# Kernel tuning notes

Measured on AMD Instinct MI355X. Metric: run time of the kernel, lower is better.

The kernel has to match this reference:

```python
import jax, jax.numpy as jnp
import numpy as np

EPS = 1e-6
MAX_ITER = 3

def skew(w):
    z = jnp.zeros_like(w[:, 0])
    return jnp.stack([
        jnp.stack([z, -w[:, 2], w[:, 1]], -1),
        jnp.stack([w[:, 2], z, -w[:, 0]], -1),
        jnp.stack([-w[:, 1], w[:, 0], z], -1)], -2)

def twist2mat(w):
    # Rodrigues formula, w: [B,3] -> R: [B,3,3]
    theta = jnp.linalg.norm(w, axis=-1, keepdims=True) + 1e-12
    axis = w / theta
    Km = skew(axis)
    th = theta[..., None]
    I = jnp.eye(3, dtype=w.dtype)
    return I + jnp.sin(th) * Km + (1.0 - jnp.cos(th)) * (Km @ Km)

def sobel_gradient(img, normalize=True):
    # replicate-pad + 3x3 Sobel, img: [B,C,H,W]
    p = jnp.pad(img, ((0, 0), (0, 0), (1, 1), (1, 1)), mode='edge')
    tl = p[..., :-2, :-2]; tc = p[..., :-2, 1:-1]; tr = p[..., :-2, 2:]
    ml = p[..., 1:-1, :-2]; mr = p[..., 1:-1, 2:]
    bl = p[..., 2:, :-2]; bc = p[..., 2:, 1:-1]; br = p[..., 2:, 2:]
    dx = (tr - tl) + 2.0 * (mr - ml) + (br - bl)
    dy = (bl - tl) + 2.0 * (bc - tc) + (br - tr)
    if normalize:
        mag = jnp.sqrt(dx * dx + dy * dy + 1e-8)
        dx, dy = dx / mag, dy / mag
    return dx, dy

def _bilinear_one(F, u, v):
    # F: [C,H,W]; u,v: [H,W] pixel coords; border padding (grid_sample-like)
    C, H, W = F.shape
    u = jnp.clip(u, 0.0, W - 1.0)
    v = jnp.clip(v, 0.0, H - 1.0)
    x0 = jnp.floor(u); y0 = jnp.floor(v)
    wx = u - x0; wy = v - y0
    x0i = x0.astype(jnp.int32); y0i = y0.astype(jnp.int32)
    x1i = jnp.minimum(x0i + 1, W - 1); y1i = jnp.minimum(y0i + 1, H - 1)
    g = lambda yi, xi: F[:, yi, xi]  # advanced-index gather -> [C,H,W]
    return (g(y0i, x0i) * (1 - wx) * (1 - wy) + g(y0i, x1i) * wx * (1 - wy)
            + g(y1i, x0i) * (1 - wx) * wy + g(y1i, x1i) * wx * wy)

def warp_features(F, u, v):
    # F: [B,C,H,W]; u,v: [B,1,H,W]
    return jax.vmap(_bilinear_one)(F, u[:, 0], v[:, 0])

def generate_xy_grid(B, H, W, K):
    fx, fy, cx, cy = [K[:, i].reshape(B, 1, 1, 1) for i in range(4)]
    uu, vv = jnp.meshgrid(jnp.arange(W, dtype=K.dtype), jnp.arange(H, dtype=K.dtype))
    px = (uu[None, None] - cx) / fx
    py = (vv[None, None] - cy) / fy
    return px, py  # [B,1,H,W] each

def batch_warp_inverse_depth(px, py, invD0, R, t, K):
    B, _, H, W = px.shape
    xy1 = jnp.concatenate([px, py, jnp.ones_like(px)], 1).reshape(B, 3, -1)
    warped = R @ xy1 + t[:, :, None] * invD0.reshape(B, 1, -1)
    x_, y_, s_ = warped[:, 0], warped[:, 1], warped[:, 2]
    fx, fy, cx, cy = [K[:, i].reshape(B, 1) for i in range(4)]
    u_ = (x_ / s_ * fx + cx).reshape(B, 1, H, W)
    v_ = (y_ / s_ * fy + cy).reshape(B, 1, H, W)
    inv_z = invD0 / s_.reshape(B, 1, H, W)
    return u_, v_, inv_z

def check_occ(inv_z_buffer, invD1, u, v, thres=0.1):
    B, _, H, W = invD1.shape
    inv_z_warped = warp_features(invD1, u, v)
    inlier = inv_z_buffer > inv_z_warped - thres
    inview = (u > 0) & (u < W) & (v > 0) & (v < H)
    return ~(inlier & inview)  # [B,1,H,W] bool

def compute_jacobian_warping(invD, K, px, py):
    # linearized at origin (pose=None branch)
    B, _, H, W = invD.shape
    x = px.reshape(B, -1); y = py.reshape(B, -1); d = invD.reshape(B, -1)
    O = jnp.zeros_like(x)
    xy = x * y
    dx_dp = jnp.stack([-xy, 1.0 + x * x, -y, d, O, -d * x], -1)
    dy_dp = jnp.stack([-(1.0 + y * y), xy, x, O, d, -d * y], -1)
    fx = K[:, 0].reshape(B, 1, 1); fy = K[:, 1].reshape(B, 1, 1)
    return dx_dp * fx, dy_dp * fy  # [B,HW,6] each

def lev_mar_H(JtWJ):
    diag = jnp.eye(6, dtype=JtWJ.dtype)
    trace = jnp.trace(JtWJ, axis1=1, axis2=2)
    return JtWJ + (trace * 1e-6)[:, None, None] * diag

def forward(twist0, x0, x1, invD0, invD1, sigma0, sigma1, K):
    B, C, H, W = x0.shape
    N = H * W
    dtype = x0.dtype
    R = twist2mat(twist0[:, :3])
    t = twist0[:, 3:]
    px, py = generate_xy_grid(B, H, W, K)
    # inverse-compositional: template Jacobian precomputed once
    Jf_x, Jf_y = sobel_gradient(x0, normalize=True)
    Jx_p, Jy_p = compute_jacobian_warping(invD0, K, px, py)
    J = (Jf_x.reshape(B, C, N, 1) * Jx_p.reshape(B, 1, N, 6)
         + Jf_y.reshape(B, C, N, 1) * Jy_p.reshape(B, 1, N, 6))  # [B,C,N,6]
    for _ in range(MAX_ITER):
        u_w, v_w, inv_z = batch_warp_inverse_depth(px, py, invD0, R, t, K)
        occ = check_occ(inv_z, invD1, u_w, v_w)
        f_r = warp_features(x1, u_w, v_w)
        sigma_r = warp_features(sigma1, u_w, v_w)
        res = f_r - x0
        sigma = jnp.sqrt(sigma_r * sigma_r + sigma0 * sigma0)
        wres = jnp.where(occ, EPS, res / sigma)  # [B,C,H,W]
        valid = (~occ).reshape(B, 1, N, 1).astype(dtype)
        Jw = (J / sigma.reshape(B, C, N, 1) * valid).reshape(B, C * N, 6)
        r = jnp.where(occ, 0.0, wres).reshape(B, C * N)
        JtWJ = jnp.einsum('bnk,bnl->bkl', Jw, Jw)
        Rhs = jnp.einsum('bnk,bn->bk', Jw, r)[..., None]
        xi = jnp.linalg.solve(lev_mar_H(JtWJ), Rhs)  # [B,6,1]
        d_R = twist2mat(-xi[:, :3, 0])
        d_t = -(d_R @ xi[:, 3:])
        t = (R @ d_t)[:, :, 0] + t
        R = R @ d_R
    return jnp.concatenate([R.reshape(B, 9), t], axis=1)  # [B,12]

def setup_inputs() -> dict:
    key = jax.random.key(0)
    ks = jax.random.split(key, 7)
    B, C, H, W = 8, 16, 240, 320
    twist0 = jax.random.normal(ks[0], (B, 6), jnp.float32) * 0.01
    x0 = jax.random.normal(ks[1], (B, C, H, W), jnp.float32)
    x1 = jax.random.normal(ks[2], (B, C, H, W), jnp.float32)
    invD0 = jax.random.uniform(ks[3], (B, 1, H, W), jnp.float32, 0.1, 1.0)
    invD1 = jax.random.uniform(ks[4], (B, 1, H, W), jnp.float32, 0.1, 1.0)
    sigma0 = jax.random.uniform(ks[5], (B, C, H, W), jnp.float32, 0.1, 1.0)
    sigma1 = jax.random.uniform(ks[6], (B, C, H, W), jnp.float32, 0.1, 1.0)
    Kmat = jnp.tile(jnp.array([[0.8 * W, 0.8 * W, W / 2.0, H / 2.0]], jnp.float32), (B, 1))
    return dict(twist0=twist0, x0=x0, x1=x1, invD0=invD0, invD1=invD1,
                sigma0=sigma0, sigma1=sigma1, K=Kmat)

def reference(twist0, x0, x1, invD0, invD1, sigma0, sigma1, K):
    return forward(twist0, x0, x1, invD0, invD1, sigma0, sigma1, K)
```

## Files before the change

kernel.cpp:

```cpp
#include <hip/hip_runtime.h>
#include <hip/hip_fp16.h>

#define B_ 8
#define C_ 16
#define H_ 240
#define W_ 320
#define N_ (H_*W_)

__device__ __forceinline__ void twist2mat_dev(float w0, float w1, float w2, float R[9]) {
    float th = sqrtf(w0*w0 + w1*w1 + w2*w2) + 1e-12f;
    float ax = w0/th, ay = w1/th, az = w2/th;
    float s = sinf(th), c = cosf(th), ic = 1.0f - c;
    R[0] = 1.0f + ic*(ax*ax - 1.0f);
    R[1] = -s*az + ic*ax*ay;
    R[2] =  s*ay + ic*ax*az;
    R[3] =  s*az + ic*ax*ay;
    R[4] = 1.0f + ic*(ay*ay - 1.0f);
    R[5] = -s*ax + ic*ay*az;
    R[6] = -s*ay + ic*ax*az;
    R[7] =  s*ax + ic*ay*az;
    R[8] = 1.0f + ic*(az*az - 1.0f);
}

__device__ __forceinline__ unsigned pack_h2(float a, float b) {
    __half2 h = __floats2half2_rn(a, b);
    return *reinterpret_cast<unsigned*>(&h);
}
__device__ __forceinline__ float2 unpack_h2(unsigned u) {
    __half2 h = *reinterpret_cast<__half2*>(&u);
    return __half22float2(h);
}

__device__ __forceinline__ void solve_update(const float* __restrict__ ac, float R[9], float t[3]) {
    float M[6][7];
    {
        int idx = 0;
        #pragma unroll
        for (int k = 0; k < 6; k++)
            #pragma unroll
            for (int l = k; l < 6; l++) { M[k][l] = ac[idx]; M[l][k] = ac[idx]; idx++; }
    }
    const float trace = M[0][0]+M[1][1]+M[2][2]+M[3][3]+M[4][4]+M[5][5];
    const float lam = trace * 1e-6f;
    #pragma unroll
    for (int i = 0; i < 6; i++) { M[i][i] += lam; M[i][6] = ac[21+i]; }

    #pragma unroll
    for (int k = 0; k < 6; k++) {
        const float inv = 1.0f / M[k][k];
        #pragma unroll
        for (int i = k+1; i < 6; i++) {
            const float f = M[i][k] * inv;
            #pragma unroll
            for (int j = k; j < 7; j++) M[i][j] -= f * M[k][j];
        }
    }
    float xi[6];
    #pragma unroll
    for (int i = 5; i >= 0; i--) {
        float s = M[i][6];
        #pragma unroll
        for (int j = i+1; j < 6; j++) s -= M[i][j]*xi[j];
        xi[i] = s / M[i][i];
    }

    float dR[9];
    twist2mat_dev(-xi[0], -xi[1], -xi[2], dR);
    const float dt0 = -(dR[0]*xi[3] + dR[1]*xi[4] + dR[2]*xi[5]);
    const float dt1 = -(dR[3]*xi[3] + dR[4]*xi[4] + dR[5]*xi[5]);
    const float dt2 = -(dR[6]*xi[3] + dR[7]*xi[4] + dR[8]*xi[5]);

    const float nt0 = R[0]*dt0 + R[1]*dt1 + R[2]*dt2 + t[0];
    const float nt1 = R[3]*dt0 + R[4]*dt1 + R[5]*dt2 + t[1];
    const float nt2 = R[6]*dt0 + R[7]*dt1 + R[8]*dt2 + t[2];
    float nR[9];
    #pragma unroll
    for (int i = 0; i < 3; i++)
        #pragma unroll
        for (int j = 0; j < 3; j++)
            nR[i*3+j] = R[i*3+0]*dR[0*3+j] + R[i*3+1]*dR[1*3+j] + R[i*3+2]*dR[2*3+j];
    #pragma unroll
    for (int i = 0; i < 9; i++) R[i] = nR[i];
    t[0] = nt0; t[1] = nt1; t[2] = nt2;
}

__device__ __forceinline__ void build_RT(const float* __restrict__ twist0,
                                         const float* __restrict__ accum,
                                         int b, int iters, float R[9], float t[3]) {
    const float* w = twist0 + b*6;
    twist2mat_dev(w[0], w[1], w[2], R);
    t[0] = w[3]; t[1] = w[4]; t[2] = w[5];
    for (int j = 0; j < iters; j++)
        solve_update(accum + (size_t)(j*B_ + b)*27, R, t);
}

__launch_bounds__(256)
__global__ void precompute_kernel(const float* __restrict__ x0, const float* __restrict__ x1,
                                  const float* __restrict__ sigma0, const float* __restrict__ sigma1,
                                  uint4* __restrict__ P0h, uint4* __restrict__ X1S1h,
                                  float* __restrict__ accum)
{
    if (blockIdx.x == 0 && blockIdx.y == 0 && blockIdx.z == 0) {
        for (int k = threadIdx.x; k < 3*B_*27; k += 256) accum[k] = 0.0f;
    }
    const int pix = blockIdx.x*256 + threadIdx.x;
    const int cg = blockIdx.y;
    const int b = blockIdx.z;
    const int h = pix / W_, w = pix - h*W_;
    const int hm = max(h-1,0), hp = min(h+1,H_-1);
    const int wm = max(w-1,0), wp = min(w+1,W_-1);

    unsigned p0[8];
    unsigned xsp[4];
    #pragma unroll
    for (int i = 0; i < 4; i++) {
        const int c = cg*4 + i;
        const size_t base = ((size_t)(b*C_+c))*N_;
        const float* xc = x0 + base;
        const float tl = xc[hm*W_+wm], tc_ = xc[hm*W_+w], tr = xc[hm*W_+wp];
        const float ml = xc[h*W_+wm],                     mr = xc[h*W_+wp];
        const float bl = xc[hp*W_+wm], bc_ = xc[hp*W_+w], br = xc[hp*W_+wp];
        const float dx = tr - tl + 2.0f*(mr - ml) + (br - bl);
        const float dy = bl - tl + 2.0f*(bc_ - tc_) + (br - tr);
        const float mag = sqrtf(dx*dx + dy*dy + 1e-8f);
        const float s0v = sigma0[base + pix];
        p0[i*2+0] = pack_h2(dx/mag, dy/mag);
        p0[i*2+1] = pack_h2(xc[pix], s0v*s0v);
        xsp[i] = pack_h2(x1[base + pix], sigma1[base + pix]);
    }
    uint4 a; a.x = p0[0]; a.y = p0[1]; a.z = p0[2]; a.w = p0[3];
    uint4 bb; bb.x = p0[4]; bb.y = p0[5]; bb.z = p0[6]; bb.w = p0[7];
    P0h[((size_t)(b*8 + cg*2  ))*N_ + pix] = a;
    P0h[((size_t)(b*8 + cg*2+1))*N_ + pix] = bb;
    uint4 q; q.x = xsp[0]; q.y = xsp[1]; q.z = xsp[2]; q.w = xsp[3];
    X1S1h[((size_t)(b*4 + cg))*N_ + pix] = q;
}

__launch_bounds__(256)
__global__ void iter_kernel(const uint4* __restrict__ P0h, const uint4* __restrict__ X1S1h,
                            const float* __restrict__ invD0, const float* __restrict__ invD1,
                            const float* __restrict__ Kmat, const float* __restrict__ twist0,
                            float* __restrict__ accum, int it)
{
    const int b = blockIdx.y;
    const int pix = blockIdx.x * 256 + threadIdx.x;
    const int h = pix / W_;
    const int w = pix - h*W_;

    float Rm[9], tv[3];
    build_RT(twist0, accum, b, it, Rm, tv);

    const float fx = Kmat[b*4+0], fy = Kmat[b*4+1], cx = Kmat[b*4+2], cy = Kmat[b*4+3];

    float acc[27];
    #pragma unroll
    for (int j = 0; j < 27; j++) acc[j] = 0.0f;

    const float px = ((float)w - cx) / fx;
    const float py = ((float)h - cy) / fy;
    const float d  = invD0[b*N_ + pix];

    const float x_ = Rm[0]*px + Rm[1]*py + Rm[2] + tv[0]*d;
    const float y_ = Rm[3]*px + Rm[4]*py + Rm[5] + tv[1]*d;
    const float s_ = Rm[6]*px + Rm[7]*py + Rm[8] + tv[2]*d;
    const float u = x_/s_*fx + cx;
    const float v = y_/s_*fy + cy;
    const float inv_z = d / s_;

    const float uc = fminf(fmaxf(u, 0.0f), (float)(W_-1));
    const float vc = fminf(fmaxf(v, 0.0f), (float)(H_-1));
    const float x0f = floorf(uc), y0f = floorf(vc);
    const float wx = uc - x0f, wy = vc - y0f;
    const int x0i = (int)x0f, y0i = (int)y0f;
    const int x1i = min(x0i+1, W_-1), y1i = min(y0i+1, H_-1);
    const float w00 = (1.0f-wx)*(1.0f-wy), w01 = wx*(1.0f-wy);
    const float w10 = (1.0f-wx)*wy,        w11 = wx*wy;
    const int i00 = y0i*W_+x0i, i01 = y0i*W_+x1i, i10 = y1i*W_+x0i, i11 = y1i*W_+x1i;

    const float* dz = invD1 + b*N_;
    const float zw = dz[i00]*w00 + dz[i01]*w01 + dz[i10]*w10 + dz[i11]*w11;
    const bool inlier = inv_z > zw - 0.1f;
    const bool inview = (u > 0.0f) && (u < (float)W_) && (v > 0.0f) && (v < (float)H_);
    const bool valid  = inlier && inview;

    if (valid) {
        const float xy = px*py;
        const float Av[6] = { -xy*fx, (1.0f+px*px)*fx, -py*fx, d*fx, 0.0f, -d*px*fx };
        const float Bv[6] = { -(1.0f+py*py)*fy, xy*fy, px*fy, 0.0f, d*fy, -d*py*fy };

        float Swxx=0.f, Swxy=0.f, Swyy=0.f, Srx=0.f, Sry=0.f;
        const uint4* P0b   = P0h   + (size_t)b*8*N_;
        const uint4* X1S1b = X1S1h + (size_t)b*4*N_;

#define CH(gword, xword, t00, t01, t10, t11) { \
        const float2 g  = unpack_h2(gword); \
        const float2 xs = unpack_h2(xword); \
        const float2 a00 = unpack_h2(t00), a01 = unpack_h2(t01), \
                     a10 = unpack_h2(t10), a11 = unpack_h2(t11); \
        const float fr = a00.x*w00 + a01.x*w01 + a10.x*w10 + a11.x*w11; \
        const float sr = a00.y*w00 + a01.y*w01 + a10.y*w10 + a11.y*w11; \
        const float inv_s2 = 1.0f/(sr*sr + xs.y); \
        const float res = fr - xs.x; \
        const float gxw = g.x*inv_s2, gyw = g.y*inv_s2; \
        Swxx += g.x*gxw; Swxy += g.x*gyw; Swyy += g.y*gyw; \
        Srx  += res*gxw; Sry  += res*gyw; }

        #pragma unroll
        for (int cg = 0; cg < 4; cg++) {
            const uint4 pA = P0b[(size_t)(cg*2  )*N_ + pix];
            const uint4 pB = P0b[(size_t)(cg*2+1)*N_ + pix];
            const uint4* xsb = X1S1b + (size_t)cg*N_;
            const uint4 q00 = xsb[i00], q01 = xsb[i01], q10 = xsb[i10], q11 = xsb[i11];
            CH(pA.x, pA.y, q00.x, q01.x, q10.x, q11.x)
            CH(pA.z, pA.w, q00.y, q01.y, q10.y, q11.y)
            CH(pB.x, pB.y, q00.z, q01.z, q10.z, q11.z)
            CH(pB.z, pB.w, q00.w, q01.w, q10.w, q11.w)
        }
#undef CH

        int idx = 0;
        #pragma unroll
        for (int k = 0; k < 6; k++) {
            #pragma unroll
            for (int l = k; l < 6; l++) {
                acc[idx++] = Swxx*Av[k]*Av[l] + Swxy*(Av[k]*Bv[l] + Bv[k]*Av[l]) + Swyy*Bv[k]*Bv[l];
            }
        }
        #pragma unroll
        for (int k = 0; k < 6; k++) acc[21+k] = Srx*Av[k] + Sry*Bv[k];
    }

    const int lane = threadIdx.x & 63;
    const int wave = threadIdx.x >> 6;
    __shared__ float red[4][27];
    #pragma unroll
    for (int j = 0; j < 27; j++) {
        float vv = acc[j];
        vv += __shfl_down(vv, 32);
        vv += __shfl_down(vv, 16);
        vv += __shfl_down(vv, 8);
        vv += __shfl_down(vv, 4);
        vv += __shfl_down(vv, 2);
        vv += __shfl_down(vv, 1);
        if (lane == 0) red[wave][j] = vv;
    }
    __syncthreads();
    if (threadIdx.x < 27) {
        float s = red[0][threadIdx.x] + red[1][threadIdx.x] + red[2][threadIdx.x] + red[3][threadIdx.x];
        atomicAdd(&accum[(size_t)(it*B_ + b)*27 + threadIdx.x], s);
    }
}

__global__ void finalize_kernel(const float* __restrict__ twist0, const float* __restrict__ accum,
                                float* __restrict__ out)
{
    const int b = threadIdx.x;
    if (b >= B_) return;
    float Rm[9], tv[3];
    build_RT(twist0, accum, b, 3, Rm, tv);
    float* ob = out + b*12;
    #pragma unroll
    for (int i = 0; i < 9; i++) ob[i] = Rm[i];
    ob[9] = tv[0]; ob[10] = tv[1]; ob[11] = tv[2];
}

extern "C" void kernel_launch(void* const* d_in, const int* in_sizes, int n_in,
                              void* d_out, int out_size, void* d_ws, size_t ws_size,
                              hipStream_t stream) {
    const float* twist0 = (const float*)d_in[0];
    const float* x0     = (const float*)d_in[1];
    const float* x1     = (const float*)d_in[2];
    const float* invD0  = (const float*)d_in[3];
    const float* invD1  = (const float*)d_in[4];
    const float* sigma0 = (const float*)d_in[5];
    const float* sigma1 = (const float*)d_in[6];
    const float* Kmat   = (const float*)d_in[7];
    float* out = (float*)d_out;

    const size_t p0_bytes = (size_t)B_*8*N_*sizeof(uint4);
    const size_t xs_bytes = (size_t)B_*4*N_*sizeof(uint4);

    uint4* P0h   = (uint4*)d_ws;
    uint4* X1S1h = (uint4*)((char*)d_ws + p0_bytes);
    float* accum = (float*)((char*)d_ws + p0_bytes + xs_bytes);

    hipLaunchKernelGGL(precompute_kernel, dim3(N_/256, 4, B_), dim3(256), 0, stream,
                       x0, x1, sigma0, sigma1, P0h, X1S1h, accum);

    dim3 grid(N_/256, B_);
    for (int it = 0; it < 3; ++it) {
        hipLaunchKernelGGL(iter_kernel, grid, dim3(256), 0, stream,
                           P0h, X1S1h, invD0, invD1, Kmat, twist0, accum, it);
    }
    hipLaunchKernelGGL(finalize_kernel, dim3(1), dim3(64), 0, stream, twist0, accum, out);
}
```

Before: 362.1 us.

## Solve pose update in last block via ticket counter, drop per-block rebuild

```diff
diff --git a/kernel.cpp b/kernel.cpp
--- a/kernel.cpp
+++ b/kernel.cpp
@@ -6,6 +6,7 @@
 #define H_ 240
 #define W_ 320
 #define N_ (H_*W_)
+#define ITER_BLOCKS_PER_B (N_/256)
 
 __device__ __forceinline__ void twist2mat_dev(float w0, float w1, float w2, float R[9]) {
     float th = sqrtf(w0*w0 + w1*w1 + w2*w2) + 1e-12f;
@@ -31,19 +32,19 @@
     return __half22float2(h);
 }
 
-__device__ __forceinline__ void solve_update(const float* __restrict__ ac, float R[9], float t[3]) {
+__device__ __forceinline__ void solve_update(const float* sums, float R[9], float t[3]) {
     float M[6][7];
     {
         int idx = 0;
         #pragma unroll
         for (int k = 0; k < 6; k++)
             #pragma unroll
-            for (int l = k; l < 6; l++) { M[k][l] = ac[idx]; M[l][k] = ac[idx]; idx++; }
+            for (int l = k; l < 6; l++) { M[k][l] = sums[idx]; M[l][k] = sums[idx]; idx++; }
     }
     const float trace = M[0][0]+M[1][1]+M[2][2]+M[3][3]+M[4][4]+M[5][5];
     const float lam = trace * 1e-6f;
     #pragma unroll
-    for (int i = 0; i < 6; i++) { M[i][i] += lam; M[i][6] = ac[21+i]; }
+    for (int i = 0; i < 6; i++) { M[i][i] += lam; M[i][6] = sums[21+i]; }
 
     #pragma unroll
     for (int k = 0; k < 6; k++) {
@@ -84,24 +85,26 @@
     t[0] = nt0; t[1] = nt1; t[2] = nt2;
 }
 
-__device__ __forceinline__ void build_RT(const float* __restrict__ twist0,
-                                         const float* __restrict__ accum,
-                                         int b, int iters, float R[9], float t[3]) {
-    const float* w = twist0 + b*6;
-    twist2mat_dev(w[0], w[1], w[2], R);
-    t[0] = w[3]; t[1] = w[4]; t[2] = w[5];
-    for (int j = 0; j < iters; j++)
-        solve_update(accum + (size_t)(j*B_ + b)*27, R, t);
-}
-
 __launch_bounds__(256)
 __global__ void precompute_kernel(const float* __restrict__ x0, const float* __restrict__ x1,
                                   const float* __restrict__ sigma0, const float* __restrict__ sigma1,
+                                  const float* __restrict__ twist0,
                                   uint4* __restrict__ P0h, uint4* __restrict__ X1S1h,
-                                  float* __restrict__ accum)
+                                  float* __restrict__ accum, float* __restrict__ RTbuf,
+                                  unsigned* __restrict__ tickets)
 {
     if (blockIdx.x == 0 && blockIdx.y == 0 && blockIdx.z == 0) {
         for (int k = threadIdx.x; k < 3*B_*27; k += 256) accum[k] = 0.0f;
+        if (threadIdx.x >= 64 && threadIdx.x < 64 + 3*B_) tickets[threadIdx.x - 64] = 0u;
+        if (threadIdx.x < B_) {
+            const float* w = twist0 + threadIdx.x*6;
+            float R[9];
+            twist2mat_dev(w[0], w[1], w[2], R);
+            float* rt = RTbuf + (size_t)threadIdx.x*12;
+            #pragma unroll
+            for (int i = 0; i < 9; i++) rt[i] = R[i];
+            rt[9] = w[3]; rt[10] = w[4]; rt[11] = w[5];
+        }
     }
     const int pix = blockIdx.x*256 + threadIdx.x;
     const int cg = blockIdx.y;
@@ -110,8 +113,7 @@
     const int hm = max(h-1,0), hp = min(h+1,H_-1);
     const int wm = max(w-1,0), wp = min(w+1,W_-1);
 
-    unsigned p0[8];
-    unsigned xsp[4];
+    unsigned p0[8], xsp[4];
     #pragma unroll
     for (int i = 0; i < 4; i++) {
         const int c = cg*4 + i;
@@ -139,30 +141,29 @@
 __launch_bounds__(256)
 __global__ void iter_kernel(const uint4* __restrict__ P0h, const uint4* __restrict__ X1S1h,
                             const float* __restrict__ invD0, const float* __restrict__ invD1,
-                            const float* __restrict__ Kmat, const float* __restrict__ twist0,
-                            float* __restrict__ accum, int it)
+                            const float* __restrict__ Kmat,
+                            float* __restrict__ accum, float* __restrict__ RTbuf,
+                            unsigned* __restrict__ tickets, float* __restrict__ out, int it)
 {
     const int b = blockIdx.y;
-    const int pix = blockIdx.x * 256 + threadIdx.x;
+    const int pix = blockIdx.x*256 + threadIdx.x;
+    const int tid = threadIdx.x;
     const int h = pix / W_;
     const int w = pix - h*W_;
 
-    float Rm[9], tv[3];
-    build_RT(twist0, accum, b, it, Rm, tv);
-
+    const float* rt = RTbuf + (size_t)(it*B_ + b)*12;
+    const float R00=rt[0],R01=rt[1],R02=rt[2],R10=rt[3],R11=rt[4],R12=rt[5],
+                R20=rt[6],R21=rt[7],R22=rt[8];
+    const float t0=rt[9], t1=rt[10], t2=rt[11];
     const float fx = Kmat[b*4+0], fy = Kmat[b*4+1], cx = Kmat[b*4+2], cy = Kmat[b*4+3];
-
-    float acc[27];
-    #pragma unroll
-    for (int j = 0; j < 27; j++) acc[j] = 0.0f;
 
     const float px = ((float)w - cx) / fx;
     const float py = ((float)h - cy) / fy;
-    const float d  = invD0[b*N_ + pix];
-
-    const float x_ = Rm[0]*px + Rm[1]*py + Rm[2] + tv[0]*d;
-    const float y_ = Rm[3]*px + Rm[4]*py + Rm[5] + tv[1]*d;
-    const float s_ = Rm[6]*px + Rm[7]*py + Rm[8] + tv[2]*d;
+    const float d  = invD0[(size_t)b*N_ + pix];
+
+    const float x_ = R00*px + R01*py + R02 + t0*d;
+    const float y_ = R10*px + R11*py + R12 + t1*d;
+    const float s_ = R20*px + R21*py + R22 + t2*d;
     const float u = x_/s_*fx + cx;
     const float v = y_/s_*fy + cy;
     const float inv_z = d / s_;
@@ -177,13 +178,16 @@
     const float w10 = (1.0f-wx)*wy,        w11 = wx*wy;
     const int i00 = y0i*W_+x0i, i01 = y0i*W_+x1i, i10 = y1i*W_+x0i, i11 = y1i*W_+x1i;
 
-    const float* dz = invD1 + b*N_;
+    const float* dz = invD1 + (size_t)b*N_;
     const float zw = dz[i00]*w00 + dz[i01]*w01 + dz[i10]*w10 + dz[i11]*w11;
     const bool inlier = inv_z > zw - 0.1f;
     const bool inview = (u > 0.0f) && (u < (float)W_) && (v > 0.0f) && (v < (float)H_);
-    const bool valid  = inlier && inview;
-
-    if (valid) {
+
+    float acc[27];
+    #pragma unroll
+    for (int j = 0; j < 27; j++) acc[j] = 0.0f;
+
+    if (inlier && inview) {
         const float xy = px*py;
         const float Av[6] = { -xy*fx, (1.0f+px*px)*fx, -py*fx, d*fx, 0.0f, -d*px*fx };
         const float Bv[6] = { -(1.0f+py*py)*fy, xy*fy, px*fy, 0.0f, d*fy, -d*py*fy };
@@ -205,11 +209,11 @@
         Swxx += g.x*gxw; Swxy += g.x*gyw; Swyy += g.y*gyw; \
         Srx  += res*gxw; Sry  += res*gyw; }
 
-        #pragma unroll
-        for (int cg = 0; cg < 4; cg++) {
-            const uint4 pA = P0b[(size_t)(cg*2  )*N_ + pix];
-            const uint4 pB = P0b[(size_t)(cg*2+1)*N_ + pix];
-            const uint4* xsb = X1S1b + (size_t)cg*N_;
+        #pragma unroll 2
+        for (int cgi = 0; cgi < 4; cgi++) {
+            const uint4 pA = P0b[(size_t)(cgi*2  )*N_ + pix];
+            const uint4 pB = P0b[(size_t)(cgi*2+1)*N_ + pix];
+            const uint4* xsb = X1S1b + (size_t)cgi*N_;
             const uint4 q00 = xsb[i00], q01 = xsb[i01], q10 = xsb[i10], q11 = xsb[i11];
             CH(pA.x, pA.y, q00.x, q01.x, q10.x, q11.x)
             CH(pA.z, pA.w, q00.y, q01.y, q10.y, q11.y)
@@ -230,9 +234,9 @@
         for (int k = 0; k < 6; k++) acc[21+k] = Srx*Av[k] + Sry*Bv[k];
     }
 
-    const int lane = threadIdx.x & 63;
-    const int wave = threadIdx.x >> 6;
     __shared__ float red[4][27];
+    const int lane = tid & 63;
+    const int wave = tid >> 6;
     #pragma unroll
     for (int j = 0; j < 27; j++) {
         float vv = acc[j];
@@ -245,23 +249,42 @@
         if (lane == 0) red[wave][j] = vv;
     }
     __syncthreads();
-    if (threadIdx.x < 27) {
-        float s = red[0][threadIdx.x] + red[1][threadIdx.x] + red[2][threadIdx.x] + red[3][threadIdx.x];
-        atomicAdd(&accum[(size_t)(it*B_ + b)*27 + threadIdx.x], s);
-    }
-}
-
-__global__ void finalize_kernel(const float* __restrict__ twist0, const float* __restrict__ accum,
-                                float* __restrict__ out)
-{
-    const int b = threadIdx.x;
-    if (b >= B_) return;
-    float Rm[9], tv[3];
-    build_RT(twist0, accum, b, 3, Rm, tv);
-    float* ob = out + b*12;
-    #pragma unroll
-    for (int i = 0; i < 9; i++) ob[i] = Rm[i];
-    ob[9] = tv[0]; ob[10] = tv[1]; ob[11] = tv[2];
+    float* ac = accum + (size_t)(it*B_ + b)*27;
+    if (tid < 27) {
+        float s = red[0][tid] + red[1][tid] + red[2][tid] + red[3][tid];
+        atomicAdd(&ac[tid], s);
+    }
+    __syncthreads();
+
+    __shared__ unsigned lastFlag;
+    if (tid == 0) {
+        __threadfence();
+        unsigned prev = atomicAdd(&tickets[it*B_ + b], 1u);
+        lastFlag = (prev == ITER_BLOCKS_PER_B - 1) ? 1u : 0u;
+    }
+    __syncthreads();
+
+    if (lastFlag && tid < 64) {
+        __threadfence();
+        float sv = 0.0f;
+        if (tid < 27) sv = atomicAdd(&ac[tid], 0.0f);
+        float sums[27];
+        #pragma unroll
+        for (int j = 0; j < 27; j++) sums[j] = __shfl(sv, j);
+
+        float R[9], t[3];
+        #pragma unroll
+        for (int i = 0; i < 9; i++) R[i] = rt[i];
+        t[0] = rt[9]; t[1] = rt[10]; t[2] = rt[11];
+        solve_update(sums, R, t);
+
+        if (tid == 0) {
+            float* dst = (it == 2) ? (out + b*12) : (RTbuf + (size_t)((it+1)*B_ + b)*12);
+            #pragma unroll
+            for (int i = 0; i < 9; i++) dst[i] = R[i];
+            dst[9] = t[0]; dst[10] = t[1]; dst[11] = t[2];
+        }
+    }
 }
 
 extern "C" void kernel_launch(void* const* d_in, const int* in_sizes, int n_in,
@@ -282,15 +305,17 @@
 
     uint4* P0h   = (uint4*)d_ws;
     uint4* X1S1h = (uint4*)((char*)d_ws + p0_bytes);
-    float* accum = (float*)((char*)d_ws + p0_bytes + xs_bytes);
+    float*    accum   = (float*)((char*)d_ws + p0_bytes + xs_bytes);
+    float*    RTbuf   = accum + 3*B_*27;
+    unsigned* tickets = (unsigned*)(RTbuf + 3*B_*12);
 
     hipLaunchKernelGGL(precompute_kernel, dim3(N_/256, 4, B_), dim3(256), 0, stream,
-                       x0, x1, sigma0, sigma1, P0h, X1S1h, accum);
-
-    dim3 grid(N_/256, B_);
+                       x0, x1, sigma0, sigma1, twist0, P0h, X1S1h, accum, RTbuf, tickets);
+
+    dim3 grid(ITER_BLOCKS_PER_B, B_);
     for (int it = 0; it < 3; ++it) {
         hipLaunchKernelGGL(iter_kernel, grid, dim3(256), 0, stream,
-                           P0h, X1S1h, invD0, invD1, Kmat, twist0, accum, it);
-    }
-    hipLaunchKernelGGL(finalize_kernel, dim3(1), dim3(64), 0, stream, twist0, accum, out);
-}
+                           P0h, X1S1h, invD0, invD1, Kmat,
+                           accum, RTbuf, tickets, out, it);
+    }
+}
```

Measured after the change: 469.2 us. 29.6% more time.
